# Optimization experiments

Measured on AMD Instinct MI355X. Metric: run time of the kernel, lower is better.

## Reference

```python
import jax, jax.numpy as jnp
import numpy as np

H = 64    # n_hidden
N = 1535  # input nodes; total graph nodes Nn = N + 1
B = 32    # batch
BN_EPS = 1e-5


def _p(key, shape, scale=0.05):
    return (jax.random.normal(key, shape, dtype=jnp.float32) * scale)


def setup_inputs() -> dict:
    key = jax.random.key(0)
    ks = jax.random.split(key, 32)
    inp = {
        'input_xx': jax.random.normal(ks[0], (B, N, 8), dtype=jnp.float32),
        'input_yy': jax.random.normal(ks[1], (B, N), dtype=jnp.float32),
        'output_xx': jax.random.normal(ks[2], (B, 1, 8), dtype=jnp.float32),
        # fc1: Linear(9, H); fc2: Linear(H, H)
        'W1': _p(ks[3], (H, 9)), 'b1': _p(ks[4], (H,)),
        'W2': _p(ks[5], (H, H)), 'b2': _p(ks[6], (H,)),
        # enc_new_x: Linear(8, H)
        'Wenc': _p(ks[7], (H, 8)), 'benc': _p(ks[8], (H,)),
        # Q, K, V: Linear(H, H)
        'WQ': _p(ks[9], (H, H)), 'bQ': _p(ks[10], (H,)),
        'WK': _p(ks[11], (H, H)), 'bK': _p(ks[12], (H,)),
        'WV': _p(ks[13], (H, H)), 'bV': _p(ks[14], (H,)),
        # QK: Linear(2H, 1) split into the q-half and k-half of its weight row
        'wQKq': _p(ks[15], (H,)), 'wQKk': _p(ks[16], (H,)),
        'bQK': _p(ks[17], ()),
        # A2N: Linear(H, H)
        'WA': _p(ks[18], (H, H)), 'bA': _p(ks[19], (H,)),
        # BatchNorm1d affine params
        'gamma': jnp.ones((H,), jnp.float32), 'beta': jnp.zeros((H,), jnp.float32),
        # heads
        'Wmu': _p(ks[20], (1, H)), 'bmu': _p(ks[21], (1,)),
        'Wsig': _p(ks[22], (1, H)), 'bsig': _p(ks[23], (1,)),
    }
    return inp


def _forward(input_xx, input_yy, output_xx, W1, b1, W2, b2, Wenc, benc,
             WQ, bQ, WK, bK, WV, bV, wQKq, wQKk, bQK, WA, bA,
             gamma, beta, Wmu, bmu, Wsig, bsig):
    # encode input nodes: cat(x, y) -> fc1 -> relu -> fc2 -> relu
    x = jnp.concatenate([input_xx, input_yy[..., None]], axis=-1)  # [B,N,9]
    h = jax.nn.relu(x @ W1.T + b1)
    h = jax.nn.relu(h @ W2.T + b2)                                  # [B,N,H]
    out_enc = jax.nn.relu(output_xx[:, 0, :] @ Wenc.T + benc)       # [B,H]
    # nodes: [Nn, B, H]  (node axis first, matching the torch list of nodes)
    nodes = jnp.concatenate([jnp.transpose(h, (1, 0, 2)), out_enc[None]], axis=0)

    def communicate(nodes):
        q = nodes @ WQ.T + bQ  # [Nn,B,H]
        k = nodes @ WK.T + bK
        v = nodes @ WV.T + bV
        # QK(cat(q,k)) decomposes additively: score[i,b,j] = q[i,b].wq + k[j,b].wk + b
        sq = q @ wQKq          # [Nn,B]
        sk = k @ wQKk          # [Nn,B]
        scores = sq[:, :, None] + sk.T[None, :, :] + bQK  # [Nn,B,Nn]
        w_att = jax.nn.softmax(scores, axis=-1)
        aggre = jnp.einsum('ibj,jbh->ibh', w_att, v)      # [Nn,B,H]
        z = aggre @ WA.T + bA
        # BatchNorm1d in training mode, applied per node over the batch axis
        mu = jnp.mean(z, axis=1, keepdims=True)
        var = jnp.var(z, axis=1, keepdims=True)
        z = (z - mu) / jnp.sqrt(var + BN_EPS) * gamma + beta
        return jax.nn.relu(z)

    for _ in range(4):
        nodes = communicate(nodes)

    agg = jnp.max(nodes, axis=0)                # [B,H]
    mu_out = agg @ Wmu.T + bmu                  # [B,1]
    sig_out = (agg @ Wsig.T + bsig) ** 2 + 0.01 # [B,1]
    return mu_out, sig_out


def reference(input_xx, input_yy, output_xx, W1, b1, W2, b2, Wenc, benc,
              WQ, bQ, WK, bK, WV, bV, wQKq, wQKk, bQK, WA, bA,
              gamma, beta, Wmu, bmu, Wsig, bsig):
    return _forward(input_xx, input_yy, output_xx, W1, b1, W2, b2, Wenc, benc,
                    WQ, bQ, WK, bK, WV, bV, wQKq, wQKk, bQK, WA, bA,
                    gamma, beta, Wmu, bmu, Wsig, bsig)
```

## Files before the change

### kernel.cpp

```cpp
#include <hip/hip_runtime.h>
#include <math.h>

#define HD    64
#define NIN   1535
#define NN    1536
#define BB    32
#define BN_EPS 1e-5f
#define CH    64
#define NCH   24

#define WS_DEN 0
#define WS_NUM 768

#define STS 68

__global__ __launch_bounds__(256) void k_main(
    const float* __restrict__ xx,
    const float* __restrict__ yy,
    const float* __restrict__ oxx,
    const float* __restrict__ W1, const float* __restrict__ b1,
    const float* __restrict__ W2, const float* __restrict__ b2,
    const float* __restrict__ Wenc, const float* __restrict__ benc,
    const float* __restrict__ WK, const float* __restrict__ wQKk,
    float* __restrict__ ws) {
  __shared__ float W1s[576];
  __shared__ float b1s[64], b2s[64], bencs[64], us[64];
  __shared__ float Wencs[512];
  __shared__ float W2Ts[64 * 65];
  __shared__ float xs[512];
  __shared__ float ys[64];
  __shared__ float h1s[4][64];
  __shared__ float h2s[64 * 64];
  __shared__ float e_s[64], rbuf[256];

  const int t = threadIdx.x;
  const int blk = blockIdx.x;
  const int b = blk & 31;
  const int c = blk >> 5;
  const int pp = b * NCH + c;

  for (int e = t; e < 576; e += 256) W1s[e] = W1[e];
  for (int e = t; e < 512; e += 256) Wencs[e] = Wenc[e];
  for (int e = t; e < 4096; e += 256) {
    int h = e >> 6, k = e & 63;
    W2Ts[k * 65 + h] = W2[e];
  }
  for (int e = t; e < 512; e += 256) {
    int j = e >> 3, k = e & 7;
    int r0 = c * CH + j;
    xs[e] = (r0 < NIN) ? xx[(size_t)b * (NIN * 8) + (size_t)r0 * 8 + k]
                       : oxx[b * 8 + k];
  }
  if (t < 64) {
    b1s[t] = b1[t]; b2s[t] = b2[t]; bencs[t] = benc[t];
    int r0 = c * CH + t;
    ys[t] = (r0 < NIN) ? yy[b * NIN + r0] : 0.f;
    float a = 0.f;
    #pragma unroll
    for (int h0 = 0; h0 < 64; h0++) a += wQKk[h0] * WK[h0 * 64 + t];
    us[t] = a;
  }
  __syncthreads();

  const int w = t >> 6, lane = t & 63;
  float* h1w = h1s[w];

  float w2r[64];
  #pragma unroll
  for (int k = 0; k < 64; k++) w2r[k] = W2Ts[k * 65 + lane];

  for (int rr = 0; rr < 16; rr++) {
    int j = w * 16 + rr;
    int r0 = c * CH + j;
    const float* xr = xs + j * 8;
    float h2;
    if (r0 < NIN) {
      const float* wr = W1s + lane * 9;
      float a = b1s[lane];
      a += xr[0] * wr[0] + xr[1] * wr[1] + xr[2] * wr[2] + xr[3] * wr[3];
      a += xr[4] * wr[4] + xr[5] * wr[5] + xr[6] * wr[6] + xr[7] * wr[7];
      a += ys[j] * wr[8];
      h1w[lane] = fmaxf(a, 0.f);
      float a0 = b2s[lane], a1 = 0.f;
      #pragma unroll
      for (int k = 0; k < 64; k += 4) {
        float4 hv = *(const float4*)(h1w + k);
        a0 += hv.x * w2r[k]     + hv.z * w2r[k + 2];
        a1 += hv.y * w2r[k + 1] + hv.w * w2r[k + 3];
      }
      h2 = fmaxf(a0 + a1, 0.f);
    } else {
      const float* wr = Wencs + lane * 8;
      float a = bencs[lane];
      #pragma unroll
      for (int k = 0; k < 8; k++) a += xr[k] * wr[k];
      h2 = fmaxf(a, 0.f);
    }
    h2s[j * 64 + lane] = h2;
    float p = h2 * us[lane];
    p += __shfl_down(p, 32); p += __shfl_down(p, 16); p += __shfl_down(p, 8);
    p += __shfl_down(p, 4);  p += __shfl_down(p, 2);  p += __shfl_down(p, 1);
    if (lane == 0) e_s[j] = expf(p);
  }
  __syncthreads();

  if (t < 64) {
    float s = e_s[t];
    s += __shfl_down(s, 32); s += __shfl_down(s, 16); s += __shfl_down(s, 8);
    s += __shfl_down(s, 4);  s += __shfl_down(s, 2);  s += __shfl_down(s, 1);
    if (t == 0) ws[WS_DEN + pp] = s;
  }
  {
    float acc = 0.f;
    for (int j = w; j < 64; j += 4) acc += e_s[j] * h2s[j * 64 + lane];
    rbuf[t] = acc;
    __syncthreads();
    if (t < 64)
      ws[WS_NUM + (size_t)pp * 64 + t] =
          rbuf[t] + rbuf[64 + t] + rbuf[128 + t] + rbuf[192 + t];
  }
}

__global__ __launch_bounds__(1024) void k_post(
    const float* __restrict__ ws,
    const float* __restrict__ WV, const float* __restrict__ bV,
    const float* __restrict__ WA, const float* __restrict__ bA,
    const float* __restrict__ gamma, const float* __restrict__ beta,
    const float* __restrict__ Wmu, const float* __restrict__ bmu,
    const float* __restrict__ Wsig, const float* __restrict__ bsig,
    float* __restrict__ out) {
  __shared__ float WAs[64 * 65];
  __shared__ float WVs[4096];
  __shared__ float WAVT[4096];
  __shared__ float st[32 * STS], zs[32 * STS];
  __shared__ float bAVs[64], scs[64], shs[64];
  __shared__ float gammas[64], betas[64], wmus[64], wsigs[64], bVs[64];
  const int t = threadIdx.x;

  for (int e = t; e < 4096; e += 1024) {
    int h = e >> 6, m = e & 63;
    WAs[h * 65 + m] = WA[e];
    WVs[e] = WV[e];
  }
  if (t < 64) {
    gammas[t] = gamma[t]; betas[t] = beta[t];
    wmus[t] = Wmu[t]; wsigs[t] = Wsig[t]; bVs[t] = bV[t];
  }
  __syncthreads();

  if (t >= 512) {
    int w2 = t - 512;
    int kg = w2 >> 6;
    int h  = w2 & 63;
    float acc[8];
    #pragma unroll
    for (int j = 0; j < 8; j++) acc[j] = 0.f;
    for (int m = 0; m < 64; m++) {
      float wa = WAs[h * 65 + m];
      const float4* wv = (const float4*)(WVs + m * 64 + kg * 8);
      float4 w0 = wv[0], w1 = wv[1];
      acc[0] += wa * w0.x; acc[1] += wa * w0.y; acc[2] += wa * w0.z; acc[3] += wa * w0.w;
      acc[4] += wa * w1.x; acc[5] += wa * w1.y; acc[6] += wa * w1.z; acc[7] += wa * w1.w;
    }
    #pragma unroll
    for (int j = 0; j < 8; j++) WAVT[(kg * 8 + j) * 64 + h] = acc[j];
    if (w2 < 64) {
      float a = bA[w2];
      #pragma unroll
      for (int k = 0; k < 64; k++) a += WAs[w2 * 65 + k] * bVs[k];
      bAVs[w2] = a;
    }
  } else {
    int b2 = t >> 4, i = t & 15;
    const float* dp = ws + WS_DEN + b2 * NCH;
    float s = 0.f;
    #pragma unroll
    for (int cc = 0; cc < NCH; cc++) s += dp[cc];
    float isb = 1.0f / s;
    float a0 = 0.f, a1 = 0.f, a2 = 0.f, a3 = 0.f;
    #pragma unroll
    for (int cc = 0; cc < NCH; cc++) {
      float4 v = *(const float4*)(ws + WS_NUM +
                                  (size_t)(b2 * NCH + cc) * 64 + i * 4);
      a0 += v.x; a1 += v.y; a2 += v.z; a3 += v.w;
    }
    float* sr = st + b2 * STS + i * 4;
    sr[0] = a0 * isb; sr[1] = a1 * isb; sr[2] = a2 * isb; sr[3] = a3 * isb;
  }
  __syncthreads();

  const int bb = t >> 6;
  const int hg = t & 63;
  float wv_[64];
  #pragma unroll
  for (int k = 0; k < 64; k++) wv_[k] = WAVT[k * 64 + hg];
  const float bav = bAVs[hg];

  for (int r = 0; r < 4; r++) {
    float a0 = bav, a1 = bav;
    #pragma unroll
    for (int k = 0; k < 64; k += 4) {
      float4 v0 = *(const float4*)(st + bb * STS + k);
      float4 v1 = *(const float4*)(st + (bb + 16) * STS + k);
      a0 += v0.x * wv_[k] + v0.y * wv_[k + 1] + v0.z * wv_[k + 2] + v0.w * wv_[k + 3];
      a1 += v1.x * wv_[k] + v1.y * wv_[k + 1] + v1.z * wv_[k + 2] + v1.w * wv_[k + 3];
    }
    zs[bb * STS + hg] = a0;
    zs[(bb + 16) * STS + hg] = a1;
    __syncthreads();
    if (t < 64) {
      float s1 = 0.f;
      #pragma unroll
      for (int b2 = 0; b2 < BB; b2++) s1 += zs[b2 * STS + t];
      float mu = s1 * (1.0f / BB);
      float s2 = 0.f;
      #pragma unroll
      for (int b2 = 0; b2 < BB; b2++) {
        float d = zs[b2 * STS + t] - mu;
        s2 += d * d;
      }
      float inv = gammas[t] / sqrtf(s2 * (1.0f / BB) + BN_EPS);
      scs[t] = inv;
      shs[t] = betas[t] - mu * inv;
    }
    __syncthreads();
    for (int e = t; e < BB * 64; e += 1024) {
      int b2 = e >> 6, hh = e & 63;
      st[b2 * STS + hh] = fmaxf(zs[b2 * STS + hh] * scs[hh] + shs[hh], 0.f);
    }
    __syncthreads();
  }

  {
    int b2 = t >> 5, i = t & 31;
    float v0 = st[b2 * STS + i], v1 = st[b2 * STS + i + 32];
    float pm = v0 * wmus[i] + v1 * wmus[i + 32];
    float ps = v0 * wsigs[i] + v1 * wsigs[i + 32];
    pm += __shfl_down(pm, 16); ps += __shfl_down(ps, 16);
    pm += __shfl_down(pm, 8);  ps += __shfl_down(ps, 8);
    pm += __shfl_down(pm, 4);  ps += __shfl_down(ps, 4);
    pm += __shfl_down(pm, 2);  ps += __shfl_down(ps, 2);
    pm += __shfl_down(pm, 1);  ps += __shfl_down(ps, 1);
    if (i == 0) {
      float sg = ps + bsig[0];
      out[b2] = pm + bmu[0];
      out[BB + b2] = sg * sg + 0.01f;
    }
  }
}

extern "C" void kernel_launch(void* const* d_in, const int* in_sizes, int n_in,
                              void* d_out, int out_size, void* d_ws, size_t ws_size,
                              hipStream_t stream) {
  const float* xx   = (const float*)d_in[0];
  const float* yy   = (const float*)d_in[1];
  const float* oxx  = (const float*)d_in[2];
  const float* W1   = (const float*)d_in[3];
  const float* b1   = (const float*)d_in[4];
  const float* W2   = (const float*)d_in[5];
  const float* b2   = (const float*)d_in[6];
  const float* Wenc = (const float*)d_in[7];
  const float* benc = (const float*)d_in[8];
  const float* WK   = (const float*)d_in[11];
  const float* WV   = (const float*)d_in[13];
  const float* bV   = (const float*)d_in[14];
  const float* wQKk = (const float*)d_in[16];
  const float* WA   = (const float*)d_in[18];
  const float* bA   = (const float*)d_in[19];
  const float* gamma= (const float*)d_in[20];
  const float* beta = (const float*)d_in[21];
  const float* Wmu  = (const float*)d_in[22];
  const float* bmu  = (const float*)d_in[23];
  const float* Wsig = (const float*)d_in[24];
  const float* bsig = (const float*)d_in[25];

  float* ws  = (float*)d_ws;
  float* out = (float*)d_out;

  k_main<<<BB * NCH, 256, 0, stream>>>(xx, yy, oxx, W1, b1, W2, b2, Wenc, benc,
                                       WK, wQKk, ws);
  k_post<<<1, 1024, 0, stream>>>(ws, WV, bV, WA, bA, gamma, beta,
                                 Wmu, bmu, Wsig, bsig, out);
}
```

Baseline: 137.9 us.

## Move WA·WV weight product into an extra block of the main kernel

Adds a 769th block to k_main that computes the fused WA·WV matrix and the folded bias and writes them to workspace. k_post then only loads these precomputed values instead of computing them serially in its single block. This hides the weight-only work in parallel with the main encoder blocks. It also has each main block load its W2 row directly from global memory into registers, which drops the shared-memory transpose, and packs all shared arrays into one buffer. The cost is one more block and extra global-memory traffic.

```diff
diff --git a/kernel.cpp b/kernel.cpp
--- a/kernel.cpp
+++ b/kernel.cpp
@@ -9,10 +9,14 @@
 #define CH    64
 #define NCH   24
 
-#define WS_DEN 0
-#define WS_NUM 768
+#define WS_DEN  0
+#define WS_NUM  768
+#define WS_WAVT 49920
+#define WS_BAV  54016
 
 #define STS 68
+
+#define SMEM_F 6592
 
 __global__ __launch_bounds__(256) void k_main(
     const float* __restrict__ xx,
@@ -22,29 +26,91 @@
     const float* __restrict__ W2, const float* __restrict__ b2,
     const float* __restrict__ Wenc, const float* __restrict__ benc,
     const float* __restrict__ WK, const float* __restrict__ wQKk,
+    const float* __restrict__ WV, const float* __restrict__ bV,
+    const float* __restrict__ WA, const float* __restrict__ bA,
+    const float* __restrict__ gamma, const float* __restrict__ beta,
+    const float* __restrict__ Wmu, const float* __restrict__ Wsig,
     float* __restrict__ ws) {
-  __shared__ float W1s[576];
-  __shared__ float b1s[64], b2s[64], bencs[64], us[64];
-  __shared__ float Wencs[512];
-  __shared__ float W2Ts[64 * 65];
-  __shared__ float xs[512];
-  __shared__ float ys[64];
-  __shared__ float h1s[4][64];
-  __shared__ float h2s[64 * 64];
-  __shared__ float e_s[64], rbuf[256];
-
+  __shared__ float smem[SMEM_F];
   const int t = threadIdx.x;
   const int blk = blockIdx.x;
+
+  if (blk == 768) {
+    float* WVs = smem;
+    for (int e4 = t; e4 < 1024; e4 += 256)
+      *(float4*)(WVs + e4 * 4) = *(const float4*)(WV + e4 * 4);
+    __syncthreads();
+
+    const int kg = t >> 6, h = t & 63;
+    float4 war[16];
+    #pragma unroll
+    for (int i = 0; i < 16; i++)
+      war[i] = *(const float4*)(WA + h * 64 + i * 4);
+    float acc[16];
+    #pragma unroll
+    for (int kk = 0; kk < 16; kk++) acc[kk] = 0.f;
+    #pragma unroll
+    for (int m4 = 0; m4 < 16; m4++) {
+      float4 w4 = war[m4];
+      #pragma unroll
+      for (int s = 0; s < 4; s++) {
+        const float wa = (s == 0) ? w4.x : (s == 1) ? w4.y
+                        : (s == 2) ? w4.z : w4.w;
+        const int m = m4 * 4 + s;
+        const float4* wvp = (const float4*)(WVs + m * 64 + kg * 16);
+        float4 v0 = wvp[0], v1 = wvp[1], v2 = wvp[2], v3 = wvp[3];
+        acc[0]  += wa * v0.x; acc[1]  += wa * v0.y;
+        acc[2]  += wa * v0.z; acc[3]  += wa * v0.w;
+        acc[4]  += wa * v1.x; acc[5]  += wa * v1.y;
+        acc[6]  += wa * v1.z; acc[7]  += wa * v1.w;
+        acc[8]  += wa * v2.x; acc[9]  += wa * v2.y;
+        acc[10] += wa * v2.z; acc[11] += wa * v2.w;
+        acc[12] += wa * v3.x; acc[13] += wa * v3.y;
+        acc[14] += wa * v3.z; acc[15] += wa * v3.w;
+      }
+    }
+    #pragma unroll
+    for (int kk = 0; kk < 16; kk++)
+      ws[WS_WAVT + (size_t)(kg * 16 + kk) * 64 + h] = acc[kk];
+    if (t < 64) {
+      float a = bA[t];
+      #pragma unroll
+      for (int k = 0; k < 64; k++) a += WA[t * 64 + k] * bV[k];
+      ws[WS_BAV + t] = a;
+      float v = gamma[t] + beta[t] + Wmu[t] + Wsig[t];
+      asm volatile("" :: "v"(v));
+    }
+    return;
+  }
+
+  float* W1s   = smem;
+  float* Wencs = smem + 576;
+  float* b1s   = smem + 1088;
+  float* b2s   = smem + 1152;
+  float* bencs = smem + 1216;
+  float* us    = smem + 1280;
+  float* xs    = smem + 1344;
+  float* ys    = smem + 1856;
+  float* h1s   = smem + 1920;
+  float* e_s   = smem + 2176;
+  float* rbuf  = smem + 2240;
+  float* h2s   = smem + 2496;
+
   const int b = blk & 31;
   const int c = blk >> 5;
   const int pp = b * NCH + c;
+  const int w = t >> 6, lane = t & 63;
+
+  float w2r[64];
+  #pragma unroll
+  for (int k4 = 0; k4 < 16; k4++) {
+    float4 v = *(const float4*)(W2 + lane * 64 + k4 * 4);
+    w2r[k4 * 4]     = v.x; w2r[k4 * 4 + 1] = v.y;
+    w2r[k4 * 4 + 2] = v.z; w2r[k4 * 4 + 3] = v.w;
+  }
 
   for (int e = t; e < 576; e += 256) W1s[e] = W1[e];
   for (int e = t; e < 512; e += 256) Wencs[e] = Wenc[e];
-  for (int e = t; e < 4096; e += 256) {
-    int h = e >> 6, k = e & 63;
-    W2Ts[k * 65 + h] = W2[e];
-  }
   for (int e = t; e < 512; e += 256) {
     int j = e >> 3, k = e & 7;
     int r0 = c * CH + j;
@@ -62,12 +128,7 @@
   }
   __syncthreads();
 
-  const int w = t >> 6, lane = t & 63;
-  float* h1w = h1s[w];
-
-  float w2r[64];
-  #pragma unroll
-  for (int k = 0; k < 64; k++) w2r[k] = W2Ts[k * 65 + lane];
+  float* h1w = h1s + w * 64;
 
   for (int rr = 0; rr < 16; rr++) {
     int j = w * 16 + rr;
@@ -123,52 +184,24 @@
 
 __global__ __launch_bounds__(1024) void k_post(
     const float* __restrict__ ws,
-    const float* __restrict__ WV, const float* __restrict__ bV,
-    const float* __restrict__ WA, const float* __restrict__ bA,
     const float* __restrict__ gamma, const float* __restrict__ beta,
     const float* __restrict__ Wmu, const float* __restrict__ bmu,
     const float* __restrict__ Wsig, const float* __restrict__ bsig,
     float* __restrict__ out) {
-  __shared__ float WAs[64 * 65];
-  __shared__ float WVs[4096];
-  __shared__ float WAVT[4096];
+  __shared__ float WAVTs[4096];
   __shared__ float st[32 * STS], zs[32 * STS];
   __shared__ float bAVs[64], scs[64], shs[64];
-  __shared__ float gammas[64], betas[64], wmus[64], wsigs[64], bVs[64];
+  __shared__ float gammas[64], betas[64], wmus[64], wsigs[64];
   const int t = threadIdx.x;
 
-  for (int e = t; e < 4096; e += 1024) {
-    int h = e >> 6, m = e & 63;
-    WAs[h * 65 + m] = WA[e];
-    WVs[e] = WV[e];
-  }
-  if (t < 64) {
-    gammas[t] = gamma[t]; betas[t] = beta[t];
-    wmus[t] = Wmu[t]; wsigs[t] = Wsig[t]; bVs[t] = bV[t];
-  }
-  __syncthreads();
-
   if (t >= 512) {
-    int w2 = t - 512;
-    int kg = w2 >> 6;
-    int h  = w2 & 63;
-    float acc[8];
-    #pragma unroll
-    for (int j = 0; j < 8; j++) acc[j] = 0.f;
-    for (int m = 0; m < 64; m++) {
-      float wa = WAs[h * 65 + m];
-      const float4* wv = (const float4*)(WVs + m * 64 + kg * 8);
-      float4 w0 = wv[0], w1 = wv[1];
-      acc[0] += wa * w0.x; acc[1] += wa * w0.y; acc[2] += wa * w0.z; acc[3] += wa * w0.w;
-      acc[4] += wa * w1.x; acc[5] += wa * w1.y; acc[6] += wa * w1.z; acc[7] += wa * w1.w;
-    }
-    #pragma unroll
-    for (int j = 0; j < 8; j++) WAVT[(kg * 8 + j) * 64 + h] = acc[j];
-    if (w2 < 64) {
-      float a = bA[w2];
-      #pragma unroll
-      for (int k = 0; k < 64; k++) a += WAs[w2 * 65 + k] * bVs[k];
-      bAVs[w2] = a;
+    int u = t - 512;
+    for (int e4 = u; e4 < 1024; e4 += 512)
+      *(float4*)(WAVTs + e4 * 4) = *(const float4*)(ws + WS_WAVT + e4 * 4);
+    if (u < 64) {
+      bAVs[u]   = ws[WS_BAV + u];
+      gammas[u] = gamma[u]; betas[u] = beta[u];
+      wmus[u]   = Wmu[u];   wsigs[u] = Wsig[u];
     }
   } else {
     int b2 = t >> 4, i = t & 15;
@@ -193,7 +226,7 @@
   const int hg = t & 63;
   float wv_[64];
   #pragma unroll
-  for (int k = 0; k < 64; k++) wv_[k] = WAVT[k * 64 + hg];
+  for (int k = 0; k < 64; k++) wv_[k] = WAVTs[k * 64 + hg];
   const float bav = bAVs[hg];
 
   for (int r = 0; r < 4; r++) {
@@ -277,8 +310,8 @@
   float* ws  = (float*)d_ws;
   float* out = (float*)d_out;
 
-  k_main<<<BB * NCH, 256, 0, stream>>>(xx, yy, oxx, W1, b1, W2, b2, Wenc, benc,
-                                       WK, wQKk, ws);
-  k_post<<<1, 1024, 0, stream>>>(ws, WV, bV, WA, bA, gamma, beta,
-                                 Wmu, bmu, Wsig, bsig, out);
+  k_main<<<769, 256, 0, stream>>>(xx, yy, oxx, W1, b1, W2, b2, Wenc, benc,
+                                  WK, wQKk, WV, bV, WA, bA, gamma, beta,
+                                  Wmu, Wsig, ws);
+  k_post<<<1, 1024, 0, stream>>>(ws, gamma, beta, Wmu, bmu, Wsig, bsig, out);
 }
```

New measurement: 154.4 us. +12.0%, slower.
